# Performance work log

Measured on AMD Instinct MI355X. Metric: run time of the kernel, lower is better.

Reference implementation:

```python
import jax, jax.numpy as jnp
import numpy as np

NH, NG, NR = 128, 32, 15
NT, NS = 730, 800


def _linear_init(k, fan_in, fan_out):
    k1, k2 = jax.random.split(k)
    lim = 1.0 / np.sqrt(fan_in)
    w = jax.random.uniform(k1, (fan_in, fan_out), jnp.float32, -lim, lim)
    b = jax.random.uniform(k2, (fan_out,), jnp.float32, -lim, lim)
    return w, b


def _mlp(x, w1, b1, w2, b2):
    # Linear -> Tanh -> (Dropout: identity in eval) -> Linear
    return jnp.tanh(x @ w1 + b1) @ w2 + b2


def setup_inputs() -> dict:
    key = jax.random.key(0)
    ks = jax.random.split(key, 8)
    x = jax.random.normal(ks[0], (NT, NS, 6), jnp.float32)
    xc = jax.random.normal(ks[1], (NS, NG), jnp.float32)
    fcW1_w, fcW1_b = _linear_init(ks[2], NG, 256)
    fcW2_w, fcW2_b = _linear_init(ks[3], 256, NH * 7)
    fcT1_w, fcT1_b = _linear_init(ks[4], 6 + NG, 256)
    fcT2_w, fcT2_b = _linear_init(ks[5], 256, NH * 3)
    fcR1_w, fcR1_b = _linear_init(ks[6], NG, 256)
    fcR2_w, fcR2_b = _linear_init(ks[7], 256, NH * NR)
    return dict(x=x, xc=xc,
                fcW1_w=fcW1_w, fcW1_b=fcW1_b, fcW2_w=fcW2_w, fcW2_b=fcW2_b,
                fcT1_w=fcT1_w, fcT1_b=fcT1_b, fcT2_w=fcT2_w, fcT2_b=fcT2_b,
                fcR1_w=fcR1_w, fcR1_b=fcR1_b, fcR2_w=fcR2_w, fcR2_b=fcR2_b)


def _waternet(x, xc, fcW1_w, fcW1_b, fcW2_w, fcW2_b,
              fcT1_w, fcT1_b, fcT2_w, fcT2_b, fcR1_w, fcR1_b, fcR2_w, fcR2_b):
    nh, nr = NH, NR
    nt, ns, _ = x.shape
    P, E, T1, T2 = x[..., 0], x[..., 1], x[..., 2], x[..., 3]

    # static parameter head: [ns, nh*7] split into 7 physical params (sepPar)
    w = _mlp(xc, fcW1_w, fcW1_b, fcW2_w, fcW2_b)
    sig = jax.nn.sigmoid
    kp = sig(w[:, 0 * nh:1 * nh])
    ks_ = sig(w[:, 1 * nh:2 * nh])
    kg = sig(w[:, 2 * nh:3 * nh]) / 10.0
    gp = sig(w[:, 3 * nh:4 * nh])
    gL = jnp.exp(w[:, 4 * nh:5 * nh]) * 2.0
    qb = jax.nn.relu(w[:, 5 * nh:6 * nh])
    ga = jax.nn.softmax(w[:, 6 * nh:7 * nh], axis=1)

    # time-varying head on [forcings ; tiled static attrs]
    xcT = jnp.concatenate([x, jnp.broadcast_to(xc[None], (nt, ns, xc.shape[-1]))], axis=-1)
    v = _mlp(xcT, fcT1_w, fcT1_b, fcT2_w, fcT2_b)  # [nt, ns, nh*3]
    # vi = hardsigmoid(2*v) = clip((2v+3)/6, 0, 1) = clip(v/3 + 0.5, 0, 1)
    vi = jnp.clip(v[..., :nh] / 3.0 + 0.5, 0.0, 1.0)
    ve = jax.nn.relu(v[..., nh:2 * nh]) * 2.0
    vm = jnp.exp(v[..., 2 * nh:3 * nh])

    wR = _mlp(xc, fcR1_w, fcR1_b, fcR2_w, fcR2_b)  # [ns, nh*nr]

    # snow fraction vf = arccos((T1+T2)/(T2-T1))/pi, clamped by temperature masks
    denom = T2 - T1
    cf = (T1 + T2) / jnp.where(denom == 0.0, 1.0, denom)
    vf = jnp.arccos(jnp.clip(cf, -0.999999, 0.999999)) / 3.1415
    vf = jnp.where(T1 >= 0.0, 0.0, vf)
    vf = jnp.where(T2 <= 0.0, 1.0, vf)

    Ps = P * vf                                 # [nt, ns] snow
    Pl = (P * (1.0 - vf))[..., None] * vi       # [nt, ns, nh] liquid
    Ev = E[..., None] * ve                      # [nt, ns, nh]

    def step(carry, inp):
        Sf, Ss, Sg = carry
        ps, pl, ev, vmk = inp
        qf = jnp.minimum(Sf + ps[:, None], vmk)
        Sf = jax.nn.relu(Sf + ps[:, None] - vmk)
        H = jax.nn.relu(Ss + pl + qf - ev)
        qp = jax.nn.relu(kp * (H - gL))
        qs = ks_ * jnp.minimum(H, gL)
        Ss = H - qp - qs
        qsg = qs * gp
        qg = kg * (Sg + qsg) + qb
        Sg = Sg - qg
        # routing conv and final ga-sum are linear, so route qp+qso+qg together
        return (Sf, Ss, Sg), qp + qs * (1.0 - gp) + qg

    z = jnp.zeros((ns, nh), x.dtype)
    _, QT = jax.lax.scan(step, (z, z, z), (Ps, Pl, Ev, vm))  # QT: [nt, ns, nh]

    # convTS: per-(site, bucket) causal FIR routing with kernel r [ns, nh, nr]
    r = jax.nn.relu(wR).reshape(ns, nh, nr)
    xpad = jnp.pad(QT, ((nr - 1, 0), (0, 0), (0, 0)))
    QR = jnp.zeros_like(QT)
    for i in range(nr):  # small fixed nr taps
        QR = QR + xpad[nr - 1 - i:nr - 1 - i + nt] * r[:, :, i]

    return jnp.sum(QR * ga, axis=2)  # [nt, ns]


def reference(x, xc, fcW1_w, fcW1_b, fcW2_w, fcW2_b,
              fcT1_w, fcT1_b, fcT2_w, fcT2_b, fcR1_w, fcR1_b, fcR2_w, fcR2_b):
    return _waternet(x, xc, fcW1_w, fcW1_b, fcW2_w, fcW2_b,
                     fcT1_w, fcT1_b, fcT2_w, fcT2_b, fcR1_w, fcR1_b, fcR2_w, fcR2_b)
```

## Files before the change

### kernel.cpp

```cpp
#include <hip/hip_runtime.h>
#include <cmath>

#define NHID 128
#define NSITE 800
#define NTIME 730
#define NRTAP 15
constexpr int NSH = NSITE * NHID;

typedef _Float16 f16x8 __attribute__((ext_vector_type(8)));
typedef float f32x4 __attribute__((ext_vector_type(4)));

__device__ __forceinline__ float tanh_fast(float x) {
    float e = __expf(2.0f * x);
    return 1.0f - 2.0f / (e + 1.0f);
}
__device__ __forceinline__ float sigmoid_fast(float x) {
    return 1.0f / (1.0f + __expf(-x));
}
__device__ __forceinline__ unsigned short h_bits(_Float16 h) {
    union { _Float16 h; unsigned short u; } c; c.h = h; return c.u;
}
__device__ __forceinline__ float h_val(unsigned short u) {
    union { unsigned short u; _Float16 h; } c; c.u = u; return (float)c.h;
}
__device__ __forceinline__ int ah_swz32(int jg, int r) {
    return jg * 32 + ((r & ~7) | ((r ^ jg) & 7));
}

__global__ void k_prep_w2h(const float* __restrict__ w2, _Float16* __restrict__ w2s)
{
    int idx = blockIdx.x * 256 + threadIdx.x;
    if (idx >= 98304) return;
    int k = idx / 384, col = idx - k * 384;
    int K0 = k >> 5, kg = (k >> 3) & 3, e = k & 7;
    w2s[(size_t)K0 * 12288 + kg * 3072 + col * 8 + e] = (_Float16)w2[(size_t)k * 384 + col];
}

__global__ void k_site_l1(const float* __restrict__ xc,
                          const float* __restrict__ w1W, const float* __restrict__ b1W,
                          const float* __restrict__ w1R, const float* __restrict__ b1R,
                          const float* __restrict__ w1T, const float* __restrict__ b1T,
                          float* __restrict__ h1w, float* __restrict__ h1r,
                          float* __restrict__ basec)
{
    __shared__ float xr[32];
    int s = blockIdx.x, j = threadIdx.x;
    if (j < 32) xr[j] = xc[s * 32 + j];
    __syncthreads();
    float aW = b1W[j], aR = b1R[j], aT = b1T[j];
#pragma unroll 8
    for (int k = 0; k < 32; ++k) {
        float xv = xr[k];
        aW = fmaf(xv, w1W[k * 256 + j], aW);
        aR = fmaf(xv, w1R[k * 256 + j], aR);
        aT = fmaf(xv, w1T[(6 + k) * 256 + j], aT);
    }
    h1w[s * 256 + j]   = tanh_fast(aW);
    h1r[s * 256 + j]   = tanh_fast(aR);
    basec[s * 256 + j] = aT;
}

__global__ void k_whead(const float* __restrict__ h1w,
                        const float* __restrict__ w2, const float* __restrict__ b2,
                        float* __restrict__ params)
{
    __shared__ float h[8 * 256];
    int sBase = blockIdx.x * 8, g = blockIdx.y, tid = threadIdx.x;
    for (int p = tid; p < 2048; p += 128) h[p] = h1w[sBase * 256 + p];
    __syncthreads();
    float bias = b2[g * 128 + tid];
    float acc[8];
#pragma unroll
    for (int i = 0; i < 8; ++i) acc[i] = bias;
    for (int k = 0; k < 256; ++k) {
        float wv = w2[k * 896 + g * 128 + tid];
#pragma unroll
        for (int i = 0; i < 8; ++i) acc[i] = fmaf(h[i * 256 + k], wv, acc[i]);
    }
#pragma unroll
    for (int i = 0; i < 8; ++i) {
        float v = acc[i], o;
        if (g == 0 || g == 1 || g == 3)  o = sigmoid_fast(v);
        else if (g == 2)                 o = sigmoid_fast(v) * 0.1f;
        else if (g == 4)                 o = __expf(v) * 2.0f;
        else if (g == 5)                 o = fmaxf(v, 0.0f);
        else                             o = v;
        params[g * NSH + (sBase + i) * 128 + tid] = o;
    }
}

__global__ void k_softmax_ga(float* __restrict__ ga)
{
    int s = blockIdx.x, h = threadIdx.x;
    float v = ga[s * 128 + h];
    float m = v;
#pragma unroll
    for (int off = 32; off; off >>= 1) m = fmaxf(m, __shfl_xor(m, off));
    __shared__ float ra[2], rb[2];
    if ((h & 63) == 0) ra[h >> 6] = m;
    __syncthreads();
    m = fmaxf(ra[0], ra[1]);
    float e = __expf(v - m);
    float t = e;
#pragma unroll
    for (int off = 32; off; off >>= 1) t += __shfl_xor(t, off);
    if ((h & 63) == 0) rb[h >> 6] = t;
    __syncthreads();
    ga[s * 128 + h] = e / (rb[0] + rb[1]);
}

__global__ void k_rhead(const float* __restrict__ h1r,
                        const float* __restrict__ w2, const float* __restrict__ b2,
                        float* __restrict__ rbuf)
{
    __shared__ float h[8 * 256];
    int sBase = blockIdx.x * 8, g = blockIdx.y, tid = threadIdx.x;
    for (int p = tid; p < 2048; p += 128) h[p] = h1r[sBase * 256 + p];
    __syncthreads();
    int c = g * 128 + tid;
    float bias = b2[c];
    float acc[8];
#pragma unroll
    for (int i = 0; i < 8; ++i) acc[i] = bias;
    for (int k = 0; k < 256; ++k) {
        float wv = w2[k * 1920 + c];
#pragma unroll
        for (int i = 0; i < 8; ++i) acc[i] = fmaf(h[i * 256 + k], wv, acc[i]);
    }
    int hh = c / 15, ii = c - hh * 15;
#pragma unroll
    for (int i = 0; i < 8; ++i)
        rbuf[ii * NSH + (sBase + i) * 128 + hh] = fmaxf(acc[i], 0.0f);
}

struct ThSm2 {
    f16x8 Ah[1024];
    float xt[32][6];
    float pls[32], evs[32], psv[32];
};

__global__ __launch_bounds__(256, 4) void k_combo4(
    const float* __restrict__ x, const float* __restrict__ w1T,
    const float* __restrict__ basec, const f16x8* __restrict__ w2B,
    const float* __restrict__ b2,
    const float* __restrict__ params, const float* __restrict__ rbuf,
    float* __restrict__ state, float* __restrict__ fut, float* __restrict__ out,
    unsigned* __restrict__ PEw, unsigned short* __restrict__ VMw,
    float* __restrict__ PSw, int t0h, int rowsH,
    const unsigned* __restrict__ PEr, const unsigned short* __restrict__ VMr,
    const float* __restrict__ PSr, int t0s, int Tcs, int isFirst, int nScan)
{
    __shared__ __align__(16) char smem[sizeof(ThSm2)];
    int tid = threadIdx.x;

    if ((int)blockIdx.x < nScan) {
        float* part = (float*)smem;
        int sl = tid >> 7, hc = tid & 127;
        int lane = tid & 63, wid = tid >> 6;
        int site = blockIdx.x * 2 + sl;
        int cell = site * 128 + hc;

        float kp  = params[0 * NSH + cell];
        float ksP = params[1 * NSH + cell];
        float kgP = params[2 * NSH + cell];
        float gp  = params[3 * NSH + cell];
        float gL  = params[4 * NSH + cell];
        float qb  = params[5 * NSH + cell];
        float ga  = params[6 * NSH + cell];
        float kq  = ksP * (1.0f - gp);

        float wr[NRTAP];
#pragma unroll
        for (int i = 0; i < NRTAP; ++i) wr[i] = ga * rbuf[i * NSH + cell];

        float Sf, Ss, Sg, f[NRTAP];
        if (isFirst) {
            Sf = Ss = Sg = 0.0f;
#pragma unroll
            for (int i = 0; i < NRTAP; ++i) f[i] = 0.0f;
        } else {
            Sf = state[cell];
            Ss = state[NSH + cell];
            Sg = state[2 * NSH + cell];
#pragma unroll
            for (int i = 0; i < NRTAP; ++i) f[i] = fut[i * NSH + cell];
        }

        const unsigned* pep = PEr + cell;
        const unsigned short* vmp = VMr + cell;

#define LD_T(PE_, VM_, PS_, T_) { int t_ = (T_); bool ok_ = t_ < Tcs;          \
        PE_ = ok_ ? pep[(size_t)t_ * NSH] : 0u;                                \
        VM_ = ok_ ? vmp[(size_t)t_ * NSH] : (unsigned short)0;                 \
        PS_ = ok_ ? PSr[(size_t)t_ * 800 + site] : 0.0f; }

        unsigned peA[4], peB[4], peC[4], peD[4];
        unsigned short vmA[4], vmB[4], vmC[4], vmD[4];
        float psA[4], psB[4], psC[4], psD[4];
#pragma unroll
        for (int i = 0; i < 4; ++i) LD_T(peA[i], vmA[i], psA[i], i)
#pragma unroll
        for (int i = 0; i < 4; ++i) LD_T(peB[i], vmB[i], psB[i], 4 + i)
#pragma unroll
        for (int i = 0; i < 4; ++i) LD_T(peC[i], vmC[i], psC[i], 8 + i)
#pragma unroll
        for (int i = 0; i < 4; ++i) LD_T(peD[i], vmD[i], psD[i], 12 + i)

        int ngroups = (Tcs + 3) >> 2;
        for (int g = 0; g < ngroups; ++g) {
            int tb = g * 4;
            unsigned peE[4]; unsigned short vmE[4]; float psE[4];
#pragma unroll
            for (int i = 0; i < 4; ++i) LD_T(peE[i], vmE[i], psE[i], tb + 16 + i)

            float cs[4];
#pragma unroll
            for (int i = 0; i < 4; ++i) {
                cs[i] = 0.0f;
                if (tb + i < Tcs) {
                    float pl = h_val((unsigned short)(peA[i] & 0xffffu));
                    float ev = h_val((unsigned short)(peA[i] >> 16));
                    float vm = h_val(vmA[i]);
                    float ps = psA[i];

                    float x1 = Sf + ps;
                    float qf = fminf(x1, vm);
                    Sf = fmaxf(x1 - vm, 0.0f);
                    float H  = fmaxf(Ss + pl + qf - ev, 0.0f);
                    float qp = fmaxf(kp * (H - gL), 0.0f);
                    float mh = fminf(H, gL);
                    float qs = ksP * mh;
                    Ss = H - qp - qs;
                    float qg = fmaf(kgP, fmaf(qs, gp, Sg), qb);
                    Sg = Sg - qg;
                    float qt = qp + kq * mh + qg;
#pragma unroll
                    for (int j = 0; j < NRTAP; ++j) f[j] = fmaf(wr[j], qt, f[j]);
                    cs[i] = f[0];
#pragma unroll
                    for (int j = 0; j < NRTAP - 1; ++j) f[j] = f[j + 1];
                    f[NRTAP - 1] = 0.0f;
                }
            }
#pragma unroll
            for (int i = 0; i < 4; ++i) {
                float c = cs[i];
#pragma unroll
                for (int off = 32; off; off >>= 1) c += __shfl_xor(c, off);
                cs[i] = c;
            }
            if (lane == 0) {
#pragma unroll
                for (int i = 0; i < 4; ++i)
                    if (tb + i < Tcs) part[wid * 128 + tb + i] = cs[i];
            }
#pragma unroll
            for (int i = 0; i < 4; ++i) {
                peA[i] = peB[i]; peB[i] = peC[i]; peC[i] = peD[i]; peD[i] = peE[i];
                vmA[i] = vmB[i]; vmB[i] = vmC[i]; vmC[i] = vmD[i]; vmD[i] = vmE[i];
                psA[i] = psB[i]; psB[i] = psC[i]; psC[i] = psD[i]; psD[i] = psE[i];
            }
        }
#undef LD_T

        state[cell]           = Sf;
        state[NSH + cell]     = Ss;
        state[2 * NSH + cell] = Sg;
#pragma unroll
        for (int i = 0; i < NRTAP; ++i) fut[i * NSH + cell] = f[i];

        __syncthreads();
        {
            int sl2 = tid >> 7, tl = tid & 127;
            for (int t = tl; t < Tcs; t += 128)
                out[(size_t)(t0s + t) * 800 + blockIdx.x * 2 + sl2] =
                    part[(sl2 * 2) * 128 + t] + part[(sl2 * 2 + 1) * 128 + t];
        }
        return;
    }

    ThSm2* sm = (ThSm2*)smem;
    int m0 = ((int)blockIdx.x - nScan) * 32;
    int wid = tid >> 6, lane = tid & 63;
    int l15 = lane & 15, l4 = lane >> 4;
    int n0w = wid * 32;

    if (tid < 32) {
        int row = m0 + tid;
        const float* xp = &x[((size_t)t0h * 800 + row) * 6];
        float P = xp[0], E = xp[1], T1 = xp[2], T2 = xp[3];
        sm->xt[tid][0] = P;  sm->xt[tid][1] = E;     sm->xt[tid][2] = T1;
        sm->xt[tid][3] = T2; sm->xt[tid][4] = xp[4]; sm->xt[tid][5] = xp[5];
        float den = T2 - T1;
        float cf = (T1 + T2) / ((den == 0.0f) ? 1.0f : den);
        cf = fminf(fmaxf(cf, -0.999999f), 0.999999f);
        float vf = acosf(cf) * (1.0f / 3.1415f);
        vf = (T1 >= 0.0f) ? 0.0f : vf;
        vf = (T2 <= 0.0f) ? 1.0f : vf;
        sm->pls[tid] = P * (1.0f - vf);
        sm->evs[tid] = E;
        sm->psv[tid] = P * vf;
        PSw[row] = P * vf;
    }
    __syncthreads();

    {
        int jg = tid & 31, rg = tid >> 5;
        int j0 = jg * 8;
        float4 wA[6], wB[6];
#pragma unroll
        for (int c = 0; c < 6; ++c) {
            wA[c] = *(const float4*)&w1T[c * 256 + j0];
            wB[c] = *(const float4*)&w1T[c * 256 + j0 + 4];
        }
#pragma unroll
        for (int rr = 0; rr < 4; ++rr) {
            int r = rg * 4 + rr;
            int srow = (m0 + r) % 800;
            const float* bp = &basec[(size_t)srow * 256 + j0];
            float4 b0 = *(const float4*)bp;
            float4 b1 = *(const float4*)(bp + 4);
            float a[8] = {b0.x, b0.y, b0.z, b0.w, b1.x, b1.y, b1.z, b1.w};
#pragma unroll
            for (int c = 0; c < 6; ++c) {
                float xv = sm->xt[r][c];
                a[0] = fmaf(xv, wA[c].x, a[0]);
                a[1] = fmaf(xv, wA[c].y, a[1]);
                a[2] = fmaf(xv, wA[c].z, a[2]);
                a[3] = fmaf(xv, wA[c].w, a[3]);
                a[4] = fmaf(xv, wB[c].x, a[4]);
                a[5] = fmaf(xv, wB[c].y, a[5]);
                a[6] = fmaf(xv, wB[c].z, a[6]);
                a[7] = fmaf(xv, wB[c].w, a[7]);
            }
            f16x8 hv;
#pragma unroll
            for (int e = 0; e < 8; ++e) hv[e] = (_Float16)tanh_fast(a[e]);
            sm->Ah[ah_swz32(jg, r)] = hv;
        }
    }
    __syncthreads();

    f32x4 acc[2][6];
#pragma unroll
    for (int ch = 0; ch < 3; ++ch)
#pragma unroll
        for (int cf = 0; cf < 2; ++cf) {
            float bb = b2[ch * 128 + n0w + cf * 16 + l15];
            acc[0][ch * 2 + cf] = (f32x4){bb, bb, bb, bb};
            acc[1][ch * 2 + cf] = (f32x4){bb, bb, bb, bb};
        }
    f16x8 bf[6], bfn[6];
#pragma unroll
    for (int ch = 0; ch < 3; ++ch)
#pragma unroll
        for (int cf = 0; cf < 2; ++cf)
            bf[ch * 2 + cf] = w2B[(size_t)l4 * 384 + ch * 128 + n0w + cf * 16 + l15];
    for (int ks = 0; ks < 8; ++ks) {
        if (ks < 7) {
#pragma unroll
            for (int ch = 0; ch < 3; ++ch)
#pragma unroll
                for (int cf = 0; cf < 2; ++cf)
                    bfn[ch * 2 + cf] = w2B[(size_t)(ks + 1) * 1536 + l4 * 384
                                           + ch * 128 + n0w + cf * 16 + l15];
        }
        f16x8 af[2];
#pragma unroll
        for (int mf = 0; mf < 2; ++mf)
            af[mf] = sm->Ah[ah_swz32(ks * 4 + l4, mf * 16 + l15)];
#pragma unroll
        for (int mf = 0; mf < 2; ++mf)
#pragma unroll
            for (int nf = 0; nf < 6; ++nf)
                acc[mf][nf] = __builtin_amdgcn_mfma_f32_16x16x32_f16(
                    af[mf], bf[nf], acc[mf][nf], 0, 0, 0);
        if (ks < 7) {
#pragma unroll
            for (int nf = 0; nf < 6; ++nf) bf[nf] = bfn[nf];
        }
    }

#pragma unroll
    for (int mf = 0; mf < 2; ++mf) {
#pragma unroll
        for (int cf = 0; cf < 2; ++cf) {
            int col = n0w + cf * 16 + l15;
#pragma unroll
            for (int rr = 0; rr < 4; ++rr) {
                int r = mf * 16 + l4 * 4 + rr;
                float vp = acc[mf][0 * 2 + cf][rr];
                float ve = acc[mf][1 * 2 + cf][rr];
                float vv = acc[mf][2 * 2 + cf][rr];
                float opl = sm->pls[r] * fminf(fmaxf(vp * (1.0f / 3.0f) + 0.5f, 0.0f), 1.0f);
                float oev = sm->evs[r] * fmaxf(ve, 0.0f) * 2.0f;
                float ovm = fminf(__expf(vv), 60000.0f);
                unsigned pe = (unsigned)h_bits((_Float16)opl)
                            | ((unsigned)h_bits((_Float16)oev) << 16);
                size_t gidx = (size_t)(m0 + r) * 128 + col;
                PEw[gidx] = pe;
                VMw[gidx] = h_bits((_Float16)ovm);
            }
        }
    }
}

extern "C" void kernel_launch(void* const* d_in, const int* in_sizes, int n_in,
                              void* d_out, int out_size, void* d_ws, size_t ws_size,
                              hipStream_t stream)
{
    const float* x      = (const float*)d_in[0];
    const float* xc     = (const float*)d_in[1];
    const float* fcW1_w = (const float*)d_in[2];
    const float* fcW1_b = (const float*)d_in[3];
    const float* fcW2_w = (const float*)d_in[4];
    const float* fcW2_b = (const float*)d_in[5];
    const float* fcT1_w = (const float*)d_in[6];
    const float* fcT1_b = (const float*)d_in[7];
    const float* fcT2_w = (const float*)d_in[8];
    const float* fcT2_b = (const float*)d_in[9];
    const float* fcR1_w = (const float*)d_in[10];
    const float* fcR1_b = (const float*)d_in[11];
    const float* fcR2_w = (const float*)d_in[12];
    const float* fcR2_b = (const float*)d_in[13];
    float* out = (float*)d_out;

    char* wsb = (char*)d_ws;
    size_t off = 0;
    float* params = (float*)(wsb + off); off += (size_t)7 * NSH * 4;
    float* rbuf   = (float*)(wsb + off); off += (size_t)NRTAP * NSH * 4;
    float* basec  = (float*)(wsb + off); off += 800 * 256 * 4;
    float* h1w    = (float*)(wsb + off); off += 800 * 256 * 4;
    float* h1r    = (float*)(wsb + off); off += 800 * 256 * 4;
    float* state  = (float*)(wsb + off); off += (size_t)3 * NSH * 4;
    float* fut    = (float*)(wsb + off); off += (size_t)NRTAP * NSH * 4;
    _Float16* w2s = (_Float16*)(wsb + off); off += 98304 * 2;
    size_t fixedB = off;

    const size_t perT = (size_t)NSH * 6 + 800 * 4;
    long avail = (long)ws_size - (long)fixedB - 4096;
    int Tc = (int)(avail / (long)(2 * perT));
    if (Tc > 128) Tc = 128;
    Tc &= ~3;
    if (Tc < 4) Tc = 4;

    unsigned*       PE0 = (unsigned*)(wsb + off);       off += (size_t)Tc * NSH * 4;
    unsigned short* VM0 = (unsigned short*)(wsb + off); off += (size_t)Tc * NSH * 2;
    float*          PS0 = (float*)(wsb + off);          off += (size_t)Tc * 800 * 4;
    unsigned*       PE1 = (unsigned*)(wsb + off);       off += (size_t)Tc * NSH * 4;
    unsigned short* VM1 = (unsigned short*)(wsb + off); off += (size_t)Tc * NSH * 2;
    float*          PS1 = (float*)(wsb + off);          off += (size_t)Tc * 800 * 4;

    k_prep_w2h<<<384, 256, 0, stream>>>(fcT2_w, w2s);
    k_site_l1<<<800, 256, 0, stream>>>(xc, fcW1_w, fcW1_b, fcR1_w, fcR1_b,
                                       fcT1_w, fcT1_b, h1w, h1r, basec);
    k_whead<<<dim3(100, 7), 128, 0, stream>>>(h1w, fcW2_w, fcW2_b, params);
    k_softmax_ga<<<800, 128, 0, stream>>>(params + (size_t)6 * NSH);
    k_rhead<<<dim3(100, 15), 128, 0, stream>>>(h1r, fcR2_w, fcR2_b, rbuf);

    int nch = (NTIME + Tc - 1) / Tc;
    for (int c = 0; c <= nch; ++c) {
        int nScan = (c > 0) ? 400 : 0;
        int Tch = 0;
        if (c < nch) { Tch = NTIME - c * Tc; if (Tch > Tc) Tch = Tc; }
        int rowsH = Tch * 800;
        int thB = rowsH / 32;
        int grid = nScan + thB;
        if (grid == 0) continue;
        int t0s = (c - 1) * Tc;
        int Tcs = 0;
        if (c > 0) { Tcs = NTIME - t0s; if (Tcs > Tc) Tcs = Tc; }
        unsigned*       PEw = (c & 1) ? PE1 : PE0;
        unsigned short* VMw = (c & 1) ? VM1 : VM0;
        float*          PSw = (c & 1) ? PS1 : PS0;
        const unsigned*       PEr = ((c - 1) & 1) ? PE1 : PE0;
        const unsigned short* VMr = ((c - 1) & 1) ? VM1 : VM0;
        const float*          PSr = ((c - 1) & 1) ? PS1 : PS0;
        k_combo4<<<grid, 256, 0, stream>>>(
            x, fcT1_w, basec, (const f16x8*)w2s, fcT2_b, params, rbuf,
            state, fut, out,
            PEw, VMw, PSw, c * Tc, rowsH,
            PEr, VMr, PSr, t0s, Tcs, (c == 1) ? 1 : 0, nScan);
    }
}
```

Measured before the change: 482.1 us.

## Use 512-thread blocks, 64-row GEMM tiles, and pack P/E/VM into uint2

The fused scan-plus-MLP kernel now runs with 512 threads per block. Scan blocks each handle four sites, and the time-head GEMM tile covers 64 rows, with each wave owning 16 columns across 4 row fragments. The separate 32-bit PE and 16-bit VM staging buffers merge into one 8-byte uint2 per cell, so the scan issues a single load per step instead of two. The packed format wastes 2 bytes per cell in bandwidth and workspace. The doubled shared-memory tile and the new launch bounds may lower occupancy or reduce the available chunk length Tc.

Result: no change. 487.8 us (+1.2%).

```diff
diff --git a/kernel.cpp b/kernel.cpp
--- a/kernel.cpp
+++ b/kernel.cpp
@@ -23,8 +23,8 @@
 __device__ __forceinline__ float h_val(unsigned short u) {
     union { unsigned short u; _Float16 h; } c; c.u = u; return (float)c.h;
 }
-__device__ __forceinline__ int ah_swz32(int jg, int r) {
-    return jg * 32 + ((r & ~7) | ((r ^ jg) & 7));
+__device__ __forceinline__ int ah_swz(int jg, int r) {
+    return jg * 64 + ((r & ~7) | ((r ^ jg) & 7));
 }
 
 __global__ void k_prep_w2h(const float* __restrict__ w2, _Float16* __restrict__ w2s)
@@ -133,31 +133,30 @@
         rbuf[ii * NSH + (sBase + i) * 128 + hh] = fmaxf(acc[i], 0.0f);
 }
 
-struct ThSm2 {
-    f16x8 Ah[1024];
-    float xt[32][6];
-    float pls[32], evs[32], psv[32];
+struct ThSm3 {
+    f16x8 Ah[2048];
+    float xt[64][6];
+    float pls[64], evs[64], psv[64];
 };
 
-__global__ __launch_bounds__(256, 4) void k_combo4(
+__global__ __launch_bounds__(512, 2) void k_combo5(
     const float* __restrict__ x, const float* __restrict__ w1T,
     const float* __restrict__ basec, const f16x8* __restrict__ w2B,
     const float* __restrict__ b2,
     const float* __restrict__ params, const float* __restrict__ rbuf,
     float* __restrict__ state, float* __restrict__ fut, float* __restrict__ out,
-    unsigned* __restrict__ PEw, unsigned short* __restrict__ VMw,
-    float* __restrict__ PSw, int t0h, int rowsH,
-    const unsigned* __restrict__ PEr, const unsigned short* __restrict__ VMr,
-    const float* __restrict__ PSr, int t0s, int Tcs, int isFirst, int nScan)
-{
-    __shared__ __align__(16) char smem[sizeof(ThSm2)];
+    uint2* __restrict__ PVw, float* __restrict__ PSw, int t0h, int rowsH,
+    const uint2* __restrict__ PVr, const float* __restrict__ PSr,
+    int t0s, int Tcs, int isFirst, int nScan)
+{
+    __shared__ __align__(16) char smem[sizeof(ThSm3)];
     int tid = threadIdx.x;
 
     if ((int)blockIdx.x < nScan) {
         float* part = (float*)smem;
         int sl = tid >> 7, hc = tid & 127;
         int lane = tid & 63, wid = tid >> 6;
-        int site = blockIdx.x * 2 + sl;
+        int site = blockIdx.x * 4 + sl;
         int cell = site * 128 + hc;
 
         float kp  = params[0 * NSH + cell];
@@ -186,41 +185,39 @@
             for (int i = 0; i < NRTAP; ++i) f[i] = fut[i * NSH + cell];
         }
 
-        const unsigned* pep = PEr + cell;
-        const unsigned short* vmp = VMr + cell;
-
-#define LD_T(PE_, VM_, PS_, T_) { int t_ = (T_); bool ok_ = t_ < Tcs;          \
-        PE_ = ok_ ? pep[(size_t)t_ * NSH] : 0u;                                \
-        VM_ = ok_ ? vmp[(size_t)t_ * NSH] : (unsigned short)0;                 \
+        const uint2* pvp = PVr + cell;
+        const uint2 zz = make_uint2(0u, 0u);
+
+#define LD_T(PV_, PS_, T_) { int t_ = (T_); bool ok_ = t_ < Tcs;               \
+        PV_ = ok_ ? pvp[(size_t)t_ * NSH] : zz;                                \
         PS_ = ok_ ? PSr[(size_t)t_ * 800 + site] : 0.0f; }
 
-        unsigned peA[4], peB[4], peC[4], peD[4];
-        unsigned short vmA[4], vmB[4], vmC[4], vmD[4];
+        uint2 pvA[4], pvB[4], pvC[4], pvD[4];
         float psA[4], psB[4], psC[4], psD[4];
 #pragma unroll
-        for (int i = 0; i < 4; ++i) LD_T(peA[i], vmA[i], psA[i], i)
-#pragma unroll
-        for (int i = 0; i < 4; ++i) LD_T(peB[i], vmB[i], psB[i], 4 + i)
-#pragma unroll
-        for (int i = 0; i < 4; ++i) LD_T(peC[i], vmC[i], psC[i], 8 + i)
-#pragma unroll
-        for (int i = 0; i < 4; ++i) LD_T(peD[i], vmD[i], psD[i], 12 + i)
+        for (int i = 0; i < 4; ++i) LD_T(pvA[i], psA[i], i)
+#pragma unroll
+        for (int i = 0; i < 4; ++i) LD_T(pvB[i], psB[i], 4 + i)
+#pragma unroll
+        for (int i = 0; i < 4; ++i) LD_T(pvC[i], psC[i], 8 + i)
+#pragma unroll
+        for (int i = 0; i < 4; ++i) LD_T(pvD[i], psD[i], 12 + i)
 
         int ngroups = (Tcs + 3) >> 2;
         for (int g = 0; g < ngroups; ++g) {
             int tb = g * 4;
-            unsigned peE[4]; unsigned short vmE[4]; float psE[4];
-#pragma unroll
-            for (int i = 0; i < 4; ++i) LD_T(peE[i], vmE[i], psE[i], tb + 16 + i)
+            uint2 pvE[4]; float psE[4];
+#pragma unroll
+            for (int i = 0; i < 4; ++i) LD_T(pvE[i], psE[i], tb + 16 + i)
 
             float cs[4];
 #pragma unroll
             for (int i = 0; i < 4; ++i) {
                 cs[i] = 0.0f;
                 if (tb + i < Tcs) {
-                    float pl = h_val((unsigned short)(peA[i] & 0xffffu));
-                    float ev = h_val((unsigned short)(peA[i] >> 16));
-                    float vm = h_val(vmA[i]);
+                    float pl = h_val((unsigned short)(pvA[i].x & 0xffffu));
+                    float ev = h_val((unsigned short)(pvA[i].x >> 16));
+                    float vm = h_val((unsigned short)(pvA[i].y & 0xffffu));
                     float ps = psA[i];
 
                     float x1 = Sf + ps;
@@ -256,8 +253,7 @@
             }
 #pragma unroll
             for (int i = 0; i < 4; ++i) {
-                peA[i] = peB[i]; peB[i] = peC[i]; peC[i] = peD[i]; peD[i] = peE[i];
-                vmA[i] = vmB[i]; vmB[i] = vmC[i]; vmC[i] = vmD[i]; vmD[i] = vmE[i];
+                pvA[i] = pvB[i]; pvB[i] = pvC[i]; pvC[i] = pvD[i]; pvD[i] = pvE[i];
                 psA[i] = psB[i]; psB[i] = psC[i]; psC[i] = psD[i]; psD[i] = psE[i];
             }
         }
@@ -273,19 +269,19 @@
         {
             int sl2 = tid >> 7, tl = tid & 127;
             for (int t = tl; t < Tcs; t += 128)
-                out[(size_t)(t0s + t) * 800 + blockIdx.x * 2 + sl2] =
+                out[(size_t)(t0s + t) * 800 + blockIdx.x * 4 + sl2] =
                     part[(sl2 * 2) * 128 + t] + part[(sl2 * 2 + 1) * 128 + t];
         }
         return;
     }
 
-    ThSm2* sm = (ThSm2*)smem;
-    int m0 = ((int)blockIdx.x - nScan) * 32;
+    ThSm3* sm = (ThSm3*)smem;
+    int m0 = ((int)blockIdx.x - nScan) * 64;
     int wid = tid >> 6, lane = tid & 63;
     int l15 = lane & 15, l4 = lane >> 4;
-    int n0w = wid * 32;
-
-    if (tid < 32) {
+    int n0w = wid * 16;
+
+    if (tid < 64) {
         int row = m0 + tid;
         const float* xp = &x[((size_t)t0h * 800 + row) * 6];
         float P = xp[0], E = xp[1], T1 = xp[2], T2 = xp[3];
@@ -336,71 +332,61 @@
             f16x8 hv;
 #pragma unroll
             for (int e = 0; e < 8; ++e) hv[e] = (_Float16)tanh_fast(a[e]);
-            sm->Ah[ah_swz32(jg, r)] = hv;
-        }
-    }
-    __syncthreads();
-
-    f32x4 acc[2][6];
+            sm->Ah[ah_swz(jg, r)] = hv;
+        }
+    }
+    __syncthreads();
+
+    f32x4 acc[4][3];
+#pragma unroll
+    for (int ch = 0; ch < 3; ++ch) {
+        float bb = b2[ch * 128 + n0w + l15];
+#pragma unroll
+        for (int mf = 0; mf < 4; ++mf) acc[mf][ch] = (f32x4){bb, bb, bb, bb};
+    }
+    f16x8 bf[3], bfn[3];
 #pragma unroll
     for (int ch = 0; ch < 3; ++ch)
-#pragma unroll
-        for (int cf = 0; cf < 2; ++cf) {
-            float bb = b2[ch * 128 + n0w + cf * 16 + l15];
-            acc[0][ch * 2 + cf] = (f32x4){bb, bb, bb, bb};
-            acc[1][ch * 2 + cf] = (f32x4){bb, bb, bb, bb};
-        }
-    f16x8 bf[6], bfn[6];
-#pragma unroll
-    for (int ch = 0; ch < 3; ++ch)
-#pragma unroll
-        for (int cf = 0; cf < 2; ++cf)
-            bf[ch * 2 + cf] = w2B[(size_t)l4 * 384 + ch * 128 + n0w + cf * 16 + l15];
+        bf[ch] = w2B[(size_t)l4 * 384 + ch * 128 + n0w + l15];
     for (int ks = 0; ks < 8; ++ks) {
         if (ks < 7) {
 #pragma unroll
             for (int ch = 0; ch < 3; ++ch)
-#pragma unroll
-                for (int cf = 0; cf < 2; ++cf)
-                    bfn[ch * 2 + cf] = w2B[(size_t)(ks + 1) * 1536 + l4 * 384
-                                           + ch * 128 + n0w + cf * 16 + l15];
-        }
-        f16x8 af[2];
-#pragma unroll
-        for (int mf = 0; mf < 2; ++mf)
-            af[mf] = sm->Ah[ah_swz32(ks * 4 + l4, mf * 16 + l15)];
-#pragma unroll
-        for (int mf = 0; mf < 2; ++mf)
-#pragma unroll
-            for (int nf = 0; nf < 6; ++nf)
-                acc[mf][nf] = __builtin_amdgcn_mfma_f32_16x16x32_f16(
-                    af[mf], bf[nf], acc[mf][nf], 0, 0, 0);
+                bfn[ch] = w2B[(size_t)(ks + 1) * 1536 + l4 * 384 + ch * 128 + n0w + l15];
+        }
+        f16x8 af[4];
+#pragma unroll
+        for (int mf = 0; mf < 4; ++mf)
+            af[mf] = sm->Ah[ah_swz(ks * 4 + l4, mf * 16 + l15)];
+#pragma unroll
+        for (int mf = 0; mf < 4; ++mf)
+#pragma unroll
+            for (int ch = 0; ch < 3; ++ch)
+                acc[mf][ch] = __builtin_amdgcn_mfma_f32_16x16x32_f16(
+                    af[mf], bf[ch], acc[mf][ch], 0, 0, 0);
         if (ks < 7) {
 #pragma unroll
-            for (int nf = 0; nf < 6; ++nf) bf[nf] = bfn[nf];
-        }
-    }
-
-#pragma unroll
-    for (int mf = 0; mf < 2; ++mf) {
-#pragma unroll
-        for (int cf = 0; cf < 2; ++cf) {
-            int col = n0w + cf * 16 + l15;
-#pragma unroll
-            for (int rr = 0; rr < 4; ++rr) {
-                int r = mf * 16 + l4 * 4 + rr;
-                float vp = acc[mf][0 * 2 + cf][rr];
-                float ve = acc[mf][1 * 2 + cf][rr];
-                float vv = acc[mf][2 * 2 + cf][rr];
-                float opl = sm->pls[r] * fminf(fmaxf(vp * (1.0f / 3.0f) + 0.5f, 0.0f), 1.0f);
-                float oev = sm->evs[r] * fmaxf(ve, 0.0f) * 2.0f;
-                float ovm = fminf(__expf(vv), 60000.0f);
-                unsigned pe = (unsigned)h_bits((_Float16)opl)
-                            | ((unsigned)h_bits((_Float16)oev) << 16);
-                size_t gidx = (size_t)(m0 + r) * 128 + col;
-                PEw[gidx] = pe;
-                VMw[gidx] = h_bits((_Float16)ovm);
-            }
+            for (int ch = 0; ch < 3; ++ch) bf[ch] = bfn[ch];
+        }
+    }
+
+    int col = n0w + l15;
+#pragma unroll
+    for (int mf = 0; mf < 4; ++mf) {
+#pragma unroll
+        for (int rr = 0; rr < 4; ++rr) {
+            int r = mf * 16 + l4 * 4 + rr;
+            float vp = acc[mf][0][rr];
+            float ve = acc[mf][1][rr];
+            float vv = acc[mf][2][rr];
+            float opl = sm->pls[r] * fminf(fmaxf(vp * (1.0f / 3.0f) + 0.5f, 0.0f), 1.0f);
+            float oev = sm->evs[r] * fmaxf(ve, 0.0f) * 2.0f;
+            float ovm = fminf(__expf(vv), 60000.0f);
+            uint2 pv;
+            pv.x = (unsigned)h_bits((_Float16)opl)
+                 | ((unsigned)h_bits((_Float16)oev) << 16);
+            pv.y = (unsigned)h_bits((_Float16)ovm);
+            PVw[(size_t)(m0 + r) * 128 + col] = pv;
         }
     }
 }
@@ -437,19 +423,17 @@
     _Float16* w2s = (_Float16*)(wsb + off); off += 98304 * 2;
     size_t fixedB = off;
 
-    const size_t perT = (size_t)NSH * 6 + 800 * 4;
+    const size_t perT = (size_t)NSH * 8 + 800 * 4;
     long avail = (long)ws_size - (long)fixedB - 4096;
     int Tc = (int)(avail / (long)(2 * perT));
     if (Tc > 128) Tc = 128;
     Tc &= ~3;
     if (Tc < 4) Tc = 4;
 
-    unsigned*       PE0 = (unsigned*)(wsb + off);       off += (size_t)Tc * NSH * 4;
-    unsigned short* VM0 = (unsigned short*)(wsb + off); off += (size_t)Tc * NSH * 2;
-    float*          PS0 = (float*)(wsb + off);          off += (size_t)Tc * 800 * 4;
-    unsigned*       PE1 = (unsigned*)(wsb + off);       off += (size_t)Tc * NSH * 4;
-    unsigned short* VM1 = (unsigned short*)(wsb + off); off += (size_t)Tc * NSH * 2;
-    float*          PS1 = (float*)(wsb + off);          off += (size_t)Tc * 800 * 4;
+    uint2* PV0 = (uint2*)(wsb + off); off += (size_t)Tc * NSH * 8;
+    float* PS0 = (float*)(wsb + off); off += (size_t)Tc * 800 * 4;
+    uint2* PV1 = (uint2*)(wsb + off); off += (size_t)Tc * NSH * 8;
+    float* PS1 = (float*)(wsb + off); off += (size_t)Tc * 800 * 4;
 
     k_prep_w2h<<<384, 256, 0, stream>>>(fcT2_w, w2s);
     k_site_l1<<<800, 256, 0, stream>>>(xc, fcW1_w, fcW1_b, fcR1_w, fcR1_b,
@@ -460,26 +444,24 @@
 
     int nch = (NTIME + Tc - 1) / Tc;
     for (int c = 0; c <= nch; ++c) {
-        int nScan = (c > 0) ? 400 : 0;
+        int nScan = (c > 0) ? 200 : 0;
         int Tch = 0;
         if (c < nch) { Tch = NTIME - c * Tc; if (Tch > Tc) Tch = Tc; }
         int rowsH = Tch * 800;
-        int thB = rowsH / 32;
+        int thB = rowsH / 64;
         int grid = nScan + thB;
         if (grid == 0) continue;
         int t0s = (c - 1) * Tc;
         int Tcs = 0;
         if (c > 0) { Tcs = NTIME - t0s; if (Tcs > Tc) Tcs = Tc; }
-        unsigned*       PEw = (c & 1) ? PE1 : PE0;
-        unsigned short* VMw = (c & 1) ? VM1 : VM0;
-        float*          PSw = (c & 1) ? PS1 : PS0;
-        const unsigned*       PEr = ((c - 1) & 1) ? PE1 : PE0;
-        const unsigned short* VMr = ((c - 1) & 1) ? VM1 : VM0;
-        const float*          PSr = ((c - 1) & 1) ? PS1 : PS0;
-        k_combo4<<<grid, 256, 0, stream>>>(
+        uint2* PVw = (c & 1) ? PV1 : PV0;
+        float* PSw = (c & 1) ? PS1 : PS0;
+        const uint2* PVr = ((c - 1) & 1) ? PV1 : PV0;
+        const float* PSr = ((c - 1) & 1) ? PS1 : PS0;
+        k_combo5<<<grid, 512, 0, stream>>>(
             x, fcT1_w, basec, (const f16x8*)w2s, fcT2_b, params, rbuf,
             state, fut, out,
-            PEw, VMw, PSw, c * Tc, rowsH,
-            PEr, VMr, PSr, t0s, Tcs, (c == 1) ? 1 : 0, nScan);
-    }
-}
+            PVw, PSw, c * Tc, rowsH,
+            PVr, PSr, t0s, Tcs, (c == 1) ? 1 : 0, nScan);
+    }
+}
```
